# Kernel tuning notes

Hardware: AMD Instinct MI355X
Metric: run time of the kernel (lower is better)

Reference implementation:

```python
import jax, jax.numpy as jnp
import numpy as np

N_HEAD = 16
N_KV_GROUP = 4
WINDOW = 256


def setup_inputs() -> dict:
    key = jax.random.key(0)
    ks = jax.random.split(key, 5)
    B, T, C = 2, 2048, 1024
    KV = C // N_HEAD * N_KV_GROUP  # 256
    s = 0.02
    return {
        "x": jax.random.normal(ks[0], (B, T, C), jnp.float32),
        "Wq": jax.random.normal(ks[1], (C, C), jnp.float32) * s,
        "bq": jnp.zeros((C,), jnp.float32),
        "Wk": jax.random.normal(ks[2], (C, KV), jnp.float32) * s,
        "bk": jnp.zeros((KV,), jnp.float32),
        "Wv": jax.random.normal(ks[3], (C, KV), jnp.float32) * s,
        "bv": jnp.zeros((KV,), jnp.float32),
        "Wo": jax.random.normal(ks[4], (C, C), jnp.float32) * s,
        "bo": jnp.zeros((C,), jnp.float32),
    }


def reference(x, Wq, bq, Wk, bk, Wv, bv, Wo, bo):
    B, T, C = x.shape
    hd = C // N_HEAD  # head dim = 64
    n_rep = N_HEAD // N_KV_GROUP

    q = x @ Wq + bq                      # [B,T,C]
    k = x @ Wk + bk                      # [B,T,KV]
    v = x @ Wv + bv

    q = q.reshape(B, T, N_HEAD, hd).transpose(0, 2, 1, 3)       # [B,H,T,d]
    k = k.reshape(B, T, N_KV_GROUP, hd).transpose(0, 2, 1, 3)   # [B,G,T,d]
    v = v.reshape(B, T, N_KV_GROUP, hd).transpose(0, 2, 1, 3)

    # GQA: repeat_interleave kv heads along head dim
    k_rep = jnp.repeat(k, n_rep, axis=1)                         # [B,H,T,d]
    v_rep = jnp.repeat(v, n_rep, axis=1)

    att = jnp.einsum("bhqd,bhkd->bhqk", q, k_rep) / jnp.sqrt(jnp.float32(hd))

    # causal + sliding window band mask: q position i attends to j in [i-WINDOW, i]
    i = jnp.arange(T)[:, None]
    j = jnp.arange(T)[None, :]
    band = (j <= i) & (j >= i - WINDOW)                           # [T,T]
    att = jnp.where(band[None, None], att, jnp.float32(-jnp.inf))

    att = jax.nn.softmax(att, axis=-1)
    y = jnp.einsum("bhqk,bhkd->bhqd", att, v_rep)                 # [B,H,T,d]
    y = y.transpose(0, 2, 1, 3).reshape(B, T, C)
    return y @ Wo + bo
```

## Files before the change

### kernel.cpp

```cpp
#include <hip/hip_runtime.h>
#include <hip/hip_bf16.h>

#define TT 2048
#define CC 1024
#define KVD 256
#define QKVD 1536

typedef __bf16 bf16x8 __attribute__((ext_vector_type(8)));
typedef float f32x4 __attribute__((ext_vector_type(4)));

__device__ __forceinline__ void gload_lds16(const __hip_bfloat16* g, __hip_bfloat16* l) {
  __builtin_amdgcn_global_load_lds(
      (const __attribute__((address_space(1))) unsigned int*)g,
      (__attribute__((address_space(3))) unsigned int*)l, 16, 0, 0);
}


__global__ __launch_bounds__(256) void k_convert_x(const float* __restrict__ x,
                                                   __hip_bfloat16* __restrict__ xbf) {
  size_t idx = ((size_t)blockIdx.x * 256 + threadIdx.x) * 4;
  float4 v = *(const float4*)(x + idx);
  xbf[idx + 0] = __float2bfloat16(v.x);
  xbf[idx + 1] = __float2bfloat16(v.y);
  xbf[idx + 2] = __float2bfloat16(v.z);
  xbf[idx + 3] = __float2bfloat16(v.w);
}

__global__ __launch_bounds__(256) void k_pack_w(const float* __restrict__ Wq,
                                                const float* __restrict__ Wk,
                                                const float* __restrict__ Wv,
                                                const float* __restrict__ Wo,
                                                const float* __restrict__ bq,
                                                const float* __restrict__ bk,
                                                const float* __restrict__ bv,
                                                __hip_bfloat16* __restrict__ wqkvT,
                                                __hip_bfloat16* __restrict__ woT,
                                                float* __restrict__ bqkv) {
  if (blockIdx.z == 1 && blockIdx.y >= 16) {
    if (blockIdx.y == 16 && blockIdx.x == 0) {
      for (int i = threadIdx.x; i < 1536; i += 256) {
        float v;
        if (i < 1024)      v = bq[i];
        else if (i < 1280) v = bk[i - 1024];
        else               v = bv[i - 1280];
        bqkv[i] = v;
      }
    }
    return;
  }
  __shared__ float tile[64][65];
  const int k0 = blockIdx.x * 64;
  const int n0 = blockIdx.y * 64;
  const float* src;
  int ncols;
  __hip_bfloat16* dst;
  if (blockIdx.z == 0) {
    dst = wqkvT;
    if (n0 < 1024)      { src = Wq; ncols = 1024; }
    else if (n0 < 1280) { src = Wk - 1024; ncols = 256; }
    else                { src = Wv - 1280; ncols = 256; }
  } else {
    dst = woT; src = Wo; ncols = 1024;
  }
  const int rw = threadIdx.x >> 6;
  const int cl = threadIdx.x & 63;
#pragma unroll
  for (int i = 0; i < 16; ++i) {
    const int kr = rw + i * 4;
    tile[kr][cl] = src[(size_t)(k0 + kr) * ncols + n0 + cl];
  }
  __syncthreads();
#pragma unroll
  for (int i = 0; i < 16; ++i) {
    const int nr = rw + i * 4;
    dst[(size_t)(n0 + nr) * 1024 + k0 + cl] = __float2bfloat16(tile[cl][nr]);
  }
}


template <bool OUT_BF16, bool SPLIT_V>
__global__ __launch_bounds__(256, 4) void k_gemm_bt(const __hip_bfloat16* __restrict__ A,
                                                    const __hip_bfloat16* __restrict__ BT,
                                                    const float* __restrict__ bias,
                                                    void* __restrict__ C,
                                                    __hip_bfloat16* __restrict__ vtg,
                                                    int M, int N, int K) {
  __shared__ __hip_bfloat16 As[64][64];
  __shared__ __hip_bfloat16 Bs[128][64];

  const int tid  = threadIdx.x;
  const int m0   = blockIdx.y * 64;
  const int n0   = blockIdx.x * 128;
  const int w    = tid >> 6;
  const int lane = tid & 63;
  const int quad = lane >> 4;
  const int l16  = lane & 15;
  const int wm   = (w >> 1) * 32;
  const int wn   = (w & 1) * 64;

  const int dl_r = lane >> 3;
  const int dl_c = (lane & 7) ^ dl_r;

  const __hip_bfloat16* gA = A + (size_t)(m0 + w * 16 + dl_r) * K + dl_c * 8;
  const __hip_bfloat16* gB = BT + (size_t)(n0 + w * 32 + dl_r) * K + dl_c * 8;

  f32x4 acc[2][4] = {};

  const int nk = K >> 6;
  for (int kt = 0; kt < nk; ++kt) {
    const int k0 = kt << 6;
    gload_lds16(gA + k0,                 &As[w * 16][0]);
    gload_lds16(gA + k0 + (size_t)8 * K, &As[w * 16 + 8][0]);
    gload_lds16(gB + k0,                  &Bs[w * 32][0]);
    gload_lds16(gB + k0 + (size_t)8 * K,  &Bs[w * 32 + 8][0]);
    gload_lds16(gB + k0 + (size_t)16 * K, &Bs[w * 32 + 16][0]);
    gload_lds16(gB + k0 + (size_t)24 * K, &Bs[w * 32 + 24][0]);
    __syncthreads();

#pragma unroll
    for (int ks = 0; ks < 2; ++ks) {
      const int cb = (ks << 2) + quad;
      bf16x8 fa[2], fb[4];
#pragma unroll
      for (int i = 0; i < 2; ++i)
        fa[i] = *(const bf16x8*)&As[wm + i * 16 + l16][(cb ^ (l16 & 7)) << 3];
#pragma unroll
      for (int j = 0; j < 4; ++j)
        fb[j] = *(const bf16x8*)&Bs[wn + j * 16 + l16][(cb ^ (l16 & 7)) << 3];
#pragma unroll
      for (int i = 0; i < 2; ++i)
#pragma unroll
        for (int j = 0; j < 4; ++j)
          acc[i][j] = __builtin_amdgcn_mfma_f32_16x16x32_bf16(fa[i], fb[j], acc[i][j], 0, 0, 0);
    }
    __syncthreads();
  }

#pragma unroll
  for (int j = 0; j < 4; ++j) {
    const int gn = n0 + wn + j * 16 + l16;
    const float bias_v = bias[gn];
    if (SPLIT_V && gn >= 1280) {
      const int dfull = gn - 1280;
      const int gg = dfull >> 6;
      const int dd = dfull & 63;
#pragma unroll
      for (int i = 0; i < 2; ++i) {
        const int gm = m0 + wm + i * 16 + quad * 4;
        const int bb = gm >> 11;
        const int tl = gm & 2047;
        __hip_bfloat16 tmp[4];
#pragma unroll
        for (int r = 0; r < 4; ++r) tmp[r] = __float2bfloat16(acc[i][j][r] + bias_v);
        *(uint2*)(vtg + ((size_t)((bb * 4 + gg) * 64 + dd)) * TT + tl) = *(const uint2*)tmp;
      }
    } else {
#pragma unroll
      for (int i = 0; i < 2; ++i) {
        const int gmb = m0 + wm + i * 16 + quad * 4;
#pragma unroll
        for (int r = 0; r < 4; ++r) {
          const float v = acc[i][j][r] + bias_v;
          const size_t idx = (size_t)(gmb + r) * N + gn;
          if (OUT_BF16) ((__hip_bfloat16*)C)[idx] = __float2bfloat16(v);
          else          ((float*)C)[idx] = v;
        }
      }
    }
  }
}


__global__ __launch_bounds__(256) void k_attn(const __hip_bfloat16* __restrict__ qkv,
                                              const __hip_bfloat16* __restrict__ vtg,
                                              __hip_bfloat16* __restrict__ y) {
  __shared__ __hip_bfloat16 Kb[2][64][64];
  __shared__ __hip_bfloat16 Vb[2][64][64];
  __shared__ __hip_bfloat16 Ps[4][16][72];

  const int t    = threadIdx.x;
  const int w    = t >> 6;
  const int lane = t & 63;
  const int quad = lane >> 4;
  const int l16  = lane & 15;
  const int bx   = blockIdx.x;
  const int h    = blockIdx.y;
  const int b    = blockIdx.z;
  const int g    = h >> 2;
  const int i0   = bx * 64;
  const int qrow      = i0 + w * 16 + l16;
  const int my_q_base = i0 + w * 16 + quad * 4;

  const int lrow = lane >> 3;
  const int cgl  = (lane & 7) ^ lrow;

  const __hip_bfloat16* kg =
      qkv + ((size_t)(b * TT + w * 16 + lrow)) * QKVD + 1024 + g * 64 + cgl * 8;
  const __hip_bfloat16* vg =
      vtg + ((size_t)((b * 4 + g) * 64 + w * 16 + lrow)) * TT + cgl * 8;

  bf16x8 fq[2];
  {
    const __hip_bfloat16* qp = qkv + ((size_t)(b * TT + qrow)) * QKVD + h * 64 + quad * 8;
    fq[0] = *(const bf16x8*)qp;
    fq[1] = *(const bf16x8*)(qp + 32);
  }

  float l_r[4] = {0.f, 0.f, 0.f, 0.f};
  f32x4 o_acc[4] = {};
  const float EC = 0.125f * 1.44269504f;

  const int c_lo = bx >= 4 ? bx - 4 : 0;

  {
    const size_t ko = (size_t)(c_lo * 64) * QKVD;
    gload_lds16(kg + ko,                   &Kb[0][w * 16][0]);
    gload_lds16(kg + ko + (size_t)8 * QKVD, &Kb[0][w * 16 + 8][0]);
    const int vo = c_lo * 64;
    gload_lds16(vg + vo,                  &Vb[0][w * 16][0]);
    gload_lds16(vg + vo + (size_t)8 * TT, &Vb[0][w * 16 + 8][0]);
  }

  int buf = 0;
  for (int c = c_lo; c <= bx; ++c) {
    __syncthreads();
    if (c < bx) {
      const size_t ko = (size_t)((c + 1) * 64) * QKVD;
      gload_lds16(kg + ko,                    &Kb[buf ^ 1][w * 16][0]);
      gload_lds16(kg + ko + (size_t)8 * QKVD, &Kb[buf ^ 1][w * 16 + 8][0]);
      const int vo = (c + 1) * 64;
      gload_lds16(vg + vo,                  &Vb[buf ^ 1][w * 16][0]);
      gload_lds16(vg + vo + (size_t)8 * TT, &Vb[buf ^ 1][w * 16 + 8][0]);
    }

    const int jc = c * 64;

    f32x4 sacc[4] = {};
#pragma unroll
    for (int ks = 0; ks < 2; ++ks) {
      const int sw = (((ks << 2) + quad) ^ (l16 & 7)) << 3;
#pragma unroll
      for (int nt = 0; nt < 4; ++nt) {
        const bf16x8 fk = *(const bf16x8*)&Kb[buf][nt * 16 + l16][sw];
        sacc[nt] = __builtin_amdgcn_mfma_f32_16x16x32_bf16(fq[ks], fk, sacc[nt], 0, 0, 0);
      }
    }

#pragma unroll
    for (int r = 0; r < 4; ++r) {
      const int gi = my_q_base + r;
      const int lo = gi - 256;
#pragma unroll
      for (int nt = 0; nt < 4; ++nt) {
        const int key = jc + nt * 16 + l16;
        const bool valid = (key <= gi) & (key >= lo);
        const float p = valid ? exp2f(sacc[nt][r] * EC) : 0.f;
        l_r[r] += p;
        Ps[w][quad * 4 + r][nt * 16 + l16] = __float2bfloat16(p);
      }
    }

    const bf16x8 fp0 = *(const bf16x8*)&Ps[w][l16][quad * 8];
    const bf16x8 fp1 = *(const bf16x8*)&Ps[w][l16][32 + quad * 8];

#pragma unroll
    for (int ks = 0; ks < 2; ++ks) {
      const int sw = (((ks << 2) + quad) ^ (l16 & 7)) << 3;
#pragma unroll
      for (int jt = 0; jt < 4; ++jt) {
        const bf16x8 fv = *(const bf16x8*)&Vb[buf][jt * 16 + l16][sw];
        o_acc[jt] = __builtin_amdgcn_mfma_f32_16x16x32_bf16(ks == 0 ? fp0 : fp1, fv,
                                                            o_acc[jt], 0, 0, 0);
      }
    }
    buf ^= 1;
  }

#pragma unroll
  for (int r = 0; r < 4; ++r) {
#pragma unroll
    for (int d = 1; d < 16; d <<= 1) l_r[r] += __shfl_xor(l_r[r], d);
    const float inv = 1.f / l_r[r];
    __hip_bfloat16* yp = y + ((size_t)(b * TT + my_q_base + r)) * CC + h * 64 + l16;
#pragma unroll
    for (int jt = 0; jt < 4; ++jt)
      yp[jt * 16] = __float2bfloat16(o_acc[jt][r] * inv);
  }
}


extern "C" void kernel_launch(void* const* d_in, const int* in_sizes, int n_in,
                              void* d_out, int out_size, void* d_ws, size_t ws_size,
                              hipStream_t stream) {
  const float* x  = (const float*)d_in[0];
  const float* Wq = (const float*)d_in[1];
  const float* bq = (const float*)d_in[2];
  const float* Wk = (const float*)d_in[3];
  const float* bk = (const float*)d_in[4];
  const float* Wv = (const float*)d_in[5];
  const float* bv = (const float*)d_in[6];
  const float* Wo = (const float*)d_in[7];
  const float* bo = (const float*)d_in[8];
  float* out = (float*)d_out;

  char* ws = (char*)d_ws;
  const size_t M = 2 * TT;
  __hip_bfloat16* xbf   = (__hip_bfloat16*)(ws);
  __hip_bfloat16* qkv   = (__hip_bfloat16*)(ws + 8388608);
  __hip_bfloat16* ybf   = (__hip_bfloat16*)(ws + 20971520);
  __hip_bfloat16* wqkvT = (__hip_bfloat16*)(ws + 29360128);
  __hip_bfloat16* woT   = (__hip_bfloat16*)(ws + 32505856);
  float*          bqkv  = (float*)(ws + 34603008);
  __hip_bfloat16* vtg   = (__hip_bfloat16*)(ws + 34609152);

  k_convert_x<<<4096, 256, 0, stream>>>(x, xbf);
  k_pack_w<<<dim3(16, 24, 2), 256, 0, stream>>>(Wq, Wk, Wv, Wo, bq, bk, bv,
                                                wqkvT, woT, bqkv);

  k_gemm_bt<true, true><<<dim3(QKVD / 128, M / 64), 256, 0, stream>>>(
      xbf, wqkvT, bqkv, qkv, vtg, (int)M, QKVD, CC);

  k_attn<<<dim3(TT / 64, 16, 2), 256, 0, stream>>>(qkv, vtg, ybf);

  k_gemm_bt<false, false><<<dim3(CC / 128, M / 64), 256, 0, stream>>>(
      ybf, woT, bo, out, nullptr, (int)M, CC, CC);
}
```

Baseline: 147.1 us.

## Double-buffer GEMM LDS tiles and merge prep kernels into one launch

The GEMM kernel now keeps two LDS buffers for the A and B tiles. It prefetches the next K-tile with global_load_lds while MFMAs run on the current one, which removes one barrier per iteration. This doubles LDS use, so the launch-bounds occupancy hint drops from 4 to 3. Separately, the x conversion and the weight/bias packing kernels are merged into a single flat-grid launch to save one kernel launch.

```diff
diff --git a/kernel.cpp b/kernel.cpp
--- a/kernel.cpp
+++ b/kernel.cpp
@@ -16,50 +16,54 @@
 }
 
 
-__global__ __launch_bounds__(256) void k_convert_x(const float* __restrict__ x,
-                                                   __hip_bfloat16* __restrict__ xbf) {
-  size_t idx = ((size_t)blockIdx.x * 256 + threadIdx.x) * 4;
-  float4 v = *(const float4*)(x + idx);
-  xbf[idx + 0] = __float2bfloat16(v.x);
-  xbf[idx + 1] = __float2bfloat16(v.y);
-  xbf[idx + 2] = __float2bfloat16(v.z);
-  xbf[idx + 3] = __float2bfloat16(v.w);
-}
-
-__global__ __launch_bounds__(256) void k_pack_w(const float* __restrict__ Wq,
-                                                const float* __restrict__ Wk,
-                                                const float* __restrict__ Wv,
-                                                const float* __restrict__ Wo,
-                                                const float* __restrict__ bq,
-                                                const float* __restrict__ bk,
-                                                const float* __restrict__ bv,
-                                                __hip_bfloat16* __restrict__ wqkvT,
-                                                __hip_bfloat16* __restrict__ woT,
-                                                float* __restrict__ bqkv) {
-  if (blockIdx.z == 1 && blockIdx.y >= 16) {
-    if (blockIdx.y == 16 && blockIdx.x == 0) {
-      for (int i = threadIdx.x; i < 1536; i += 256) {
-        float v;
-        if (i < 1024)      v = bq[i];
-        else if (i < 1280) v = bk[i - 1024];
-        else               v = bv[i - 1280];
-        bqkv[i] = v;
-      }
-    }
+__global__ __launch_bounds__(256) void k_prep(const float* __restrict__ x,
+                                              const float* __restrict__ Wq,
+                                              const float* __restrict__ Wk,
+                                              const float* __restrict__ Wv,
+                                              const float* __restrict__ Wo,
+                                              const float* __restrict__ bq,
+                                              const float* __restrict__ bk,
+                                              const float* __restrict__ bv,
+                                              __hip_bfloat16* __restrict__ xbf,
+                                              __hip_bfloat16* __restrict__ wqkvT,
+                                              __hip_bfloat16* __restrict__ woT,
+                                              float* __restrict__ bqkv) {
+  const int bxid = blockIdx.x;
+  if (bxid < 4096) {
+    size_t idx = ((size_t)bxid * 256 + threadIdx.x) * 4;
+    float4 v = *(const float4*)(x + idx);
+    xbf[idx + 0] = __float2bfloat16(v.x);
+    xbf[idx + 1] = __float2bfloat16(v.y);
+    xbf[idx + 2] = __float2bfloat16(v.z);
+    xbf[idx + 3] = __float2bfloat16(v.w);
     return;
   }
+  if (bxid == 4736) {
+    for (int i = threadIdx.x; i < 1536; i += 256) {
+      float v;
+      if (i < 1024)      v = bq[i];
+      else if (i < 1280) v = bk[i - 1024];
+      else               v = bv[i - 1280];
+      bqkv[i] = v;
+    }
+    return;
+  }
   __shared__ float tile[64][65];
-  const int k0 = blockIdx.x * 64;
-  const int n0 = blockIdx.y * 64;
   const float* src;
-  int ncols;
+  int ncols, k0, n0;
   __hip_bfloat16* dst;
-  if (blockIdx.z == 0) {
+  if (bxid < 4480) {
+    const int idx = bxid - 4096;
+    k0 = (idx & 15) * 64;
+    n0 = (idx >> 4) * 64;
     dst = wqkvT;
     if (n0 < 1024)      { src = Wq; ncols = 1024; }
     else if (n0 < 1280) { src = Wk - 1024; ncols = 256; }
     else                { src = Wv - 1280; ncols = 256; }
   } else {
+    const int idx = bxid - 4480;
+    k0 = (idx & 15) * 64;
+    n0 = (idx >> 4) * 64;
     dst = woT; src = Wo; ncols = 1024;
   }
   const int rw = threadIdx.x >> 6;
@@ -79,14 +83,14 @@
 
 
 template <bool OUT_BF16, bool SPLIT_V>
-__global__ __launch_bounds__(256, 4) void k_gemm_bt(const __hip_bfloat16* __restrict__ A,
+__global__ __launch_bounds__(256, 3) void k_gemm_bt(const __hip_bfloat16* __restrict__ A,
                                                     const __hip_bfloat16* __restrict__ BT,
                                                     const float* __restrict__ bias,
                                                     void* __restrict__ C,
                                                     __hip_bfloat16* __restrict__ vtg,
                                                     int M, int N, int K) {
-  __shared__ __hip_bfloat16 As[64][64];
-  __shared__ __hip_bfloat16 Bs[128][64];
+  __shared__ __hip_bfloat16 As[2][64][64];
+  __shared__ __hip_bfloat16 Bs[2][128][64];
 
   const int tid  = threadIdx.x;
   const int m0   = blockIdx.y * 64;
@@ -107,15 +111,28 @@
   f32x4 acc[2][4] = {};
 
   const int nk = K >> 6;
+
+  {
+    gload_lds16(gA,                  &As[0][w * 16][0]);
+    gload_lds16(gA + (size_t)8 * K,  &As[0][w * 16 + 8][0]);
+    gload_lds16(gB,                  &Bs[0][w * 32][0]);
+    gload_lds16(gB + (size_t)8 * K,  &Bs[0][w * 32 + 8][0]);
+    gload_lds16(gB + (size_t)16 * K, &Bs[0][w * 32 + 16][0]);
+    gload_lds16(gB + (size_t)24 * K, &Bs[0][w * 32 + 24][0]);
+  }
+
+  int buf = 0;
   for (int kt = 0; kt < nk; ++kt) {
-    const int k0 = kt << 6;
-    gload_lds16(gA + k0,                 &As[w * 16][0]);
-    gload_lds16(gA + k0 + (size_t)8 * K, &As[w * 16 + 8][0]);
-    gload_lds16(gB + k0,                  &Bs[w * 32][0]);
-    gload_lds16(gB + k0 + (size_t)8 * K,  &Bs[w * 32 + 8][0]);
-    gload_lds16(gB + k0 + (size_t)16 * K, &Bs[w * 32 + 16][0]);
-    gload_lds16(gB + k0 + (size_t)24 * K, &Bs[w * 32 + 24][0]);
     __syncthreads();
+    if (kt + 1 < nk) {
+      const int k0 = (kt + 1) << 6;
+      gload_lds16(gA + k0,                  &As[buf ^ 1][w * 16][0]);
+      gload_lds16(gA + k0 + (size_t)8 * K,  &As[buf ^ 1][w * 16 + 8][0]);
+      gload_lds16(gB + k0,                  &Bs[buf ^ 1][w * 32][0]);
+      gload_lds16(gB + k0 + (size_t)8 * K,  &Bs[buf ^ 1][w * 32 + 8][0]);
+      gload_lds16(gB + k0 + (size_t)16 * K, &Bs[buf ^ 1][w * 32 + 16][0]);
+      gload_lds16(gB + k0 + (size_t)24 * K, &Bs[buf ^ 1][w * 32 + 24][0]);
+    }
 
 #pragma unroll
     for (int ks = 0; ks < 2; ++ks) {
@@ -123,17 +140,17 @@
       bf16x8 fa[2], fb[4];
 #pragma unroll
       for (int i = 0; i < 2; ++i)
-        fa[i] = *(const bf16x8*)&As[wm + i * 16 + l16][(cb ^ (l16 & 7)) << 3];
+        fa[i] = *(const bf16x8*)&As[buf][wm + i * 16 + l16][(cb ^ (l16 & 7)) << 3];
 #pragma unroll
       for (int j = 0; j < 4; ++j)
-        fb[j] = *(const bf16x8*)&Bs[wn + j * 16 + l16][(cb ^ (l16 & 7)) << 3];
+        fb[j] = *(const bf16x8*)&Bs[buf][wn + j * 16 + l16][(cb ^ (l16 & 7)) << 3];
 #pragma unroll
       for (int i = 0; i < 2; ++i)
 #pragma unroll
         for (int j = 0; j < 4; ++j)
           acc[i][j] = __builtin_amdgcn_mfma_f32_16x16x32_bf16(fa[i], fb[j], acc[i][j], 0, 0, 0);
     }
-    __syncthreads();
+    buf ^= 1;
   }
 
 #pragma unroll
@@ -214,7 +231,7 @@
 
   {
     const size_t ko = (size_t)(c_lo * 64) * QKVD;
-    gload_lds16(kg + ko,                   &Kb[0][w * 16][0]);
+    gload_lds16(kg + ko,                    &Kb[0][w * 16][0]);
     gload_lds16(kg + ko + (size_t)8 * QKVD, &Kb[0][w * 16 + 8][0]);
     const int vo = c_lo * 64;
     gload_lds16(vg + vo,                  &Vb[0][w * 16][0]);
@@ -313,9 +330,8 @@
   float*          bqkv  = (float*)(ws + 34603008);
   __hip_bfloat16* vtg   = (__hip_bfloat16*)(ws + 34609152);
 
-  k_convert_x<<<4096, 256, 0, stream>>>(x, xbf);
-  k_pack_w<<<dim3(16, 24, 2), 256, 0, stream>>>(Wq, Wk, Wv, Wo, bq, bk, bv,
-                                                wqkvT, woT, bqkv);
+  k_prep<<<4737, 256, 0, stream>>>(x, Wq, Wk, Wv, Wo, bq, bk, bv,
+                                   xbf, wqkvT, woT, bqkv);
 
   k_gemm_bt<true, true><<<dim3(QKVD / 128, M / 64), 256, 0, stream>>>(
       xbf, wqkvT, bqkv, qkv, vtg, (int)M, QKVD, CC);
```

Measured after the change: 146.6 us. Within noise of the previous version (-0.3%).
